# Kernel tuning notes

Hardware: AMD Instinct MI355X
Metric: run time of the kernel (lower is better)

The kernel has to match this reference:

```python
import jax, jax.numpy as jnp
import numpy as np

D = 1024
H = 16
HD = D // H
FFN = D * 2
EPS = 1e-5


def _layernorm(x, g, b):
    mu = jnp.mean(x, axis=-1, keepdims=True)
    var = jnp.var(x, axis=-1, keepdims=True)
    return (x - mu) * jax.lax.rsqrt(var + EPS) * g + b


def setup_inputs() -> dict:
    key = jax.random.key(0)
    ks = jax.random.split(key, 12)
    s = 1.0 / np.sqrt(D)
    inp = {
        "x": jax.random.normal(ks[0], (2, 2048, D), dtype=jnp.float32),
        "Wq": jax.random.normal(ks[1], (D, D), dtype=jnp.float32) * s,
        "bq": jnp.zeros((D,), jnp.float32),
        "Wk": jax.random.normal(ks[2], (D, D), dtype=jnp.float32) * s,
        "bk": jnp.zeros((D,), jnp.float32),
        "Wv": jax.random.normal(ks[3], (D, D), dtype=jnp.float32) * s,
        "bv": jnp.zeros((D,), jnp.float32),
        "Wo": jax.random.normal(ks[4], (D, D), dtype=jnp.float32) * s,
        "bo": jnp.zeros((D,), jnp.float32),
        "g1": jnp.ones((D,), jnp.float32),
        "b1": jnp.zeros((D,), jnp.float32),
        "W_ff1": jax.random.normal(ks[5], (D, FFN), dtype=jnp.float32) * s,
        "b_ff1": jnp.zeros((FFN,), jnp.float32),
        "W_ff2": jax.random.normal(ks[6], (FFN, D), dtype=jnp.float32) * (1.0 / np.sqrt(FFN)),
        "b_ff2": jnp.zeros((D,), jnp.float32),
        "g2": jnp.ones((D,), jnp.float32),
        "b2": jnp.zeros((D,), jnp.float32),
    }
    return inp


def reference(x, Wq, bq, Wk, bk, Wv, bv, Wo, bo, g1, b1, W_ff1, b_ff1, W_ff2, b_ff2, g2, b2):
    B, S, _ = x.shape
    # QKV projections -> [B, H, S, HD]
    def split_heads(t):
        return t.reshape(B, S, H, HD).transpose(0, 2, 1, 3)
    Q = split_heads(x @ Wq + bq)
    K = split_heads(x @ Wk + bk)
    V = split_heads(x @ Wv + bv)
    scores = jnp.einsum('bhqd,bhkd->bhqk', Q, K) / np.sqrt(HD).astype(np.float32)
    attn = jax.nn.softmax(scores, axis=-1)  # dropout = identity in eval
    ctx = jnp.einsum('bhqk,bhkd->bhqd', attn, V)
    ctx = ctx.transpose(0, 2, 1, 3).reshape(B, S, D)
    x = _layernorm(x + ctx @ Wo + bo, g1, b1)
    h = jax.nn.gelu(x @ W_ff1 + b_ff1, approximate=False)
    x = _layernorm(x + h @ W_ff2 + b_ff2, g2, b2)
    return x
```

## Files before the change

kernel.cpp:

```cpp
#include <hip/hip_runtime.h>

#define SEQ 2048
#define NTOK 4096
#define DM 1024
#define LDQK 3072

typedef __attribute__((ext_vector_type(4))) float f32x4;
typedef __attribute__((ext_vector_type(8))) short short8;
typedef __attribute__((ext_vector_type(4))) short short4v;

__device__ __forceinline__ short f2bf(float f) {
  union { float f; unsigned u; } x; x.f = f;
  unsigned r = x.u + 0x7fffu + ((x.u >> 16) & 1u);
  return (short)(r >> 16);
}

__device__ __forceinline__ float bf2f(short s) {
  union { unsigned u; float f; } x;
  x.u = ((unsigned)(unsigned short)s) << 16;
  return x.f;
}

__device__ __forceinline__ void async_load16(const void* g, void* l) {
  __builtin_amdgcn_global_load_lds(
      (const __attribute__((address_space(1))) void*)g,
      (__attribute__((address_space(3))) void*)l, 16, 0, 0);
}

__global__ void __launch_bounds__(256) prep_all(
    const float* __restrict__ Wq, const float* __restrict__ Wk,
    const float* __restrict__ Wv, const float* __restrict__ Wo,
    const float* __restrict__ Wf1, const float* __restrict__ Wf2,
    const float* __restrict__ x,
    short* __restrict__ Wqkv, short* __restrict__ Wto,
    short* __restrict__ Wtf1, short* __restrict__ Wtf2,
    short* __restrict__ xb) {
  const int z = blockIdx.z;
  const int tx = threadIdx.x, ty = threadIdx.y;
  if (z == 6) {
    int blk = blockIdx.y * 64 + blockIdx.x;
    int i = blk * 256 + ty * 32 + tx;
    f32x4 v = ((const f32x4*)x)[i];
    short4v o;
#pragma unroll
    for (int j = 0; j < 4; ++j) o[j] = f2bf(v[j]);
    ((short4v*)xb)[i] = o;
    return;
  }
  const float* in;
  short* out;
  int K, N;
  switch (z) {
    case 0: in = Wq;  out = Wqkv;               K = 1024; N = 1024; break;
    case 1: in = Wk;  out = Wqkv + 1024 * 1024; K = 1024; N = 1024; break;
    case 2: in = Wv;  out = Wqkv + 2048 * 1024; K = 1024; N = 1024; break;
    case 3: in = Wo;  out = Wto;                K = 1024; N = 1024; break;
    case 4: in = Wf1; out = Wtf1;               K = 1024; N = 2048; break;
    default: in = Wf2; out = Wtf2;              K = 2048; N = 1024; break;
  }
  if (blockIdx.x * 32 >= N || blockIdx.y * 32 >= K) return;
  __shared__ float t[32][33];
  const int n = blockIdx.x * 32 + tx;
#pragma unroll
  for (int i = 0; i < 4; ++i) {
    int k = blockIdx.y * 32 + ty + i * 8;
    t[ty + i * 8][tx] = in[(size_t)k * N + n];
  }
  __syncthreads();
  const int k2 = blockIdx.y * 32 + tx;
#pragma unroll
  for (int i = 0; i < 4; ++i) {
    int n2 = blockIdx.x * 32 + ty + i * 8;
    out[(size_t)n2 * K + k2] = f2bf(t[tx][ty + i * 8]);
  }
}

template <int EPI, bool TRIPLE, bool DBUF>
__global__ void __launch_bounds__(256, 2) gemm_bt(
    const short* __restrict__ A, const short* __restrict__ Bt,
    const float* __restrict__ b0, const float* __restrict__ b1,
    const float* __restrict__ b2, void* __restrict__ Cout,
    short* __restrict__ VtOut, int M, int N, int K) {
  __shared__ __align__(16) short As[DBUF ? 2 * 128 * 64 : 128 * 64];
  __shared__ __align__(16) short Bs[DBUF ? 2 * 128 * 64 : 128 * 64];
  const int w = threadIdx.x >> 6, lane = threadIdx.x & 63;
  const int hi = lane >> 4, lo = lane & 15;
  const int bm = blockIdx.y, bn = blockIdx.x;
  const int wr = w >> 1, wc = w & 1;
  f32x4 acc[4][4] = {};
  const int nkt = K >> 6;

  auto stage = [&](int kt, int buf) {
#pragma unroll
    for (int j = 0; j < 4; ++j) {
      int c = (j * 4 + w) * 64 + lane;
      int r = c >> 3;
      int scc = (c & 7) ^ (r & 7);
      async_load16(A + (size_t)(bm * 128 + r) * K + kt * 64 + scc * 8,
                   &As[buf * (128 * 64) + (j * 4 + w) * 512]);
      async_load16(Bt + (size_t)(bn * 128 + r) * K + kt * 64 + scc * 8,
                   &Bs[buf * (128 * 64) + (j * 4 + w) * 512]);
    }
  };

  if (DBUF) {
    stage(0, 0);
    __syncthreads();
  }

  for (int kt = 0; kt < nkt; ++kt) {
    int buf = 0;
    if (DBUF) {
      buf = kt & 1;
      if (kt + 1 < nkt) stage(kt + 1, buf ^ 1);
    } else {
      stage(kt, 0);
      __syncthreads();
    }
#pragma unroll
    for (int ks = 0; ks < 2; ++ks) {
      short8 af[4], bf[4];
#pragma unroll
      for (int m = 0; m < 4; ++m) {
        int row = wr * 64 + m * 16 + lo;
        int ch = (ks * 4 + hi) ^ (row & 7);
        af[m] = *(const short8*)(&As[buf * (128 * 64) + row * 64 + ch * 8]);
      }
#pragma unroll
      for (int n = 0; n < 4; ++n) {
        int row = wc * 64 + n * 16 + lo;
        int ch = (ks * 4 + hi) ^ (row & 7);
        bf[n] = *(const short8*)(&Bs[buf * (128 * 64) + row * 64 + ch * 8]);
      }
#pragma unroll
      for (int m = 0; m < 4; ++m)
#pragma unroll
        for (int n = 0; n < 4; ++n)
          acc[m][n] = __builtin_amdgcn_mfma_f32_16x16x32_bf16(af[m], bf[n], acc[m][n], 0, 0, 0);
    }
    __syncthreads();
  }
  const float* bp = b0;
  if (TRIPLE) { int r = bn >> 3; bp = (r == 0) ? b0 : ((r == 1) ? b1 : b2); }
  const int colb = bn * 128 + wc * 64 + lo;
  if (TRIPLE && bn >= 16) {
#pragma unroll
    for (int m = 0; m < 4; ++m) {
      int row0 = bm * 128 + wr * 64 + m * 16 + hi * 4;
      int bb = row0 >> 11, ss = row0 & 2047;
#pragma unroll
      for (int n = 0; n < 4; ++n) {
        int col = colb + n * 16;
        int vdim = col - 2048;
        int hh = vdim >> 6, dd = vdim & 63;
        float bs = bp[vdim];
        short4v t;
#pragma unroll
        for (int j = 0; j < 4; ++j) t[j] = f2bf(acc[m][n][j] + bs);
        *(short4v*)&VtOut[((size_t)(bb * 16 + hh) * 64 + dd) * SEQ + ss] = t;
      }
    }
    return;
  }
#pragma unroll
  for (int m = 0; m < 4; ++m) {
    int row0 = bm * 128 + wr * 64 + m * 16 + hi * 4;
#pragma unroll
    for (int n = 0; n < 4; ++n) {
      int col = colb + n * 16;
      float bs = bp[TRIPLE ? (col & 1023) : col];
#pragma unroll
      for (int j = 0; j < 4; ++j) {
        float v = acc[m][n][j] + bs;
        if (EPI == 1) v = 0.5f * v * (1.f + erff(v * 0.70710678f));
        ((short*)Cout)[(size_t)(row0 + j) * N + col] = f2bf(v);
      }
    }
  }
}

__global__ void __launch_bounds__(256, 2) gemm_n64(
    const short* __restrict__ A, const short* __restrict__ Bt,
    const float* __restrict__ b0, const short* __restrict__ resid,
    short* __restrict__ Cout, int M, int N, int K) {
  __shared__ __align__(16) short As[2][128 * 64];
  __shared__ __align__(16) short Bs[2][64 * 64];
  const int w = threadIdx.x >> 6, lane = threadIdx.x & 63;
  const int hi = lane >> 4, lo = lane & 15;
  const int bm = blockIdx.y, bn = blockIdx.x;
  const int wr = w >> 1, wc = w & 1;
  f32x4 acc[4][2] = {};
  const int nkt = K >> 6;

  auto stage = [&](int kt, int buf) {
#pragma unroll
    for (int j = 0; j < 4; ++j) {
      int c = (j * 4 + w) * 64 + lane;
      int r = c >> 3;
      int scc = (c & 7) ^ (r & 7);
      async_load16(A + (size_t)(bm * 128 + r) * K + kt * 64 + scc * 8,
                   &As[buf][(j * 4 + w) * 512]);
    }
#pragma unroll
    for (int j = 0; j < 2; ++j) {
      int c = j * 256 + w * 64 + lane;
      int r = c >> 3;
      int scc = (c & 7) ^ (r & 7);
      async_load16(Bt + (size_t)(bn * 64 + r) * K + kt * 64 + scc * 8,
                   &Bs[buf][(j * 256 + w * 64) * 8]);
    }
  };

  stage(0, 0);
  __syncthreads();

  for (int kt = 0; kt < nkt; ++kt) {
    const int buf = kt & 1;
    if (kt + 1 < nkt) stage(kt + 1, buf ^ 1);
#pragma unroll
    for (int ks = 0; ks < 2; ++ks) {
      short8 af[4], bf[2];
#pragma unroll
      for (int m = 0; m < 4; ++m) {
        int row = wr * 64 + m * 16 + lo;
        int ch = (ks * 4 + hi) ^ (row & 7);
        af[m] = *(const short8*)(&As[buf][row * 64 + ch * 8]);
      }
#pragma unroll
      for (int n = 0; n < 2; ++n) {
        int row = wc * 32 + n * 16 + lo;
        int ch = (ks * 4 + hi) ^ (row & 7);
        bf[n] = *(const short8*)(&Bs[buf][row * 64 + ch * 8]);
      }
#pragma unroll
      for (int m = 0; m < 4; ++m)
#pragma unroll
        for (int n = 0; n < 2; ++n)
          acc[m][n] = __builtin_amdgcn_mfma_f32_16x16x32_bf16(af[m], bf[n], acc[m][n], 0, 0, 0);
    }
    __syncthreads();
  }
  const int colb = bn * 64 + wc * 32 + lo;
#pragma unroll
  for (int m = 0; m < 4; ++m) {
    int row0 = bm * 128 + wr * 64 + m * 16 + hi * 4;
#pragma unroll
    for (int n = 0; n < 2; ++n) {
      int col = colb + n * 16;
      float bs = b0[col];
#pragma unroll
      for (int j = 0; j < 4; ++j) {
        size_t idx = (size_t)(row0 + j) * N + col;
        Cout[idx] = f2bf(acc[m][n][j] + bs + bf2f(resid[idx]));
      }
    }
  }
}

__global__ void __launch_bounds__(256, 2) attn_kernel(
    const short* __restrict__ Qb, const short* __restrict__ Kb,
    const short* __restrict__ Vt, short* __restrict__ ctx) {
  const int w = threadIdx.x >> 6, lane = threadIdx.x & 63;
  const int hi = lane >> 4, lo = lane & 15;
  const int tid = threadIdx.x;
  const int L = blockIdx.x;
  const int W = (L & 7) * 128 + (L >> 3);
  const int qt = W & 31, bh = W >> 5;
  const int b = bh >> 4, h = bh & 15;
  const int qbase = qt * 64 + w * 16;
  const float C = 0.18033688f;

  __shared__ __align__(16) short Ks[2][64 * 64];
  __shared__ __align__(16) short Vs[2][64 * 64];
  __shared__ __align__(16) short P[4][16 * 64];

  const short* qp = Qb + (size_t)(b * SEQ + qbase + lo) * LDQK + h * 64;
  short8 bq[2];
#pragma unroll
  for (int c = 0; c < 2; ++c)
    bq[c] = *(const short8*)(qp + c * 32 + hi * 8);

  const short* kb = Kb + (size_t)(b * SEQ) * LDQK + h * 64;
  const short* vb = Vt + (size_t)bh * 64 * SEQ;

  auto stage = [&](int kt, int buf) {
    const short* kg = kb + (size_t)(kt * 64) * LDQK;
#pragma unroll
    for (int i = 0; i < 2; ++i) {
      int c = i * 256 + tid;
      int r = c >> 3, scc = (c & 7) ^ (r & 7);
      async_load16(kg + (size_t)r * LDQK + scc * 8,
                   &Ks[buf][(i * 256 + w * 64) * 8]);
    }
    const short* vg = vb + kt * 64;
#pragma unroll
    for (int i = 0; i < 2; ++i) {
      int c = i * 256 + tid;
      int r = c >> 3, sc2 = (c & 7) ^ (r & 7);
      async_load16(vg + (size_t)r * SEQ + sc2 * 8,
                   &Vs[buf][(i * 256 + w * 64) * 8]);
    }
  };

  stage(0, 0);
  __syncthreads();

  f32x4 o[4] = {};
  float lacc = 0.f;
  const int x7 = lo & 7;

  for (int kt = 0; kt < SEQ / 64; ++kt) {
    const int buf = kt & 1;
    if (kt + 1 < SEQ / 64) stage(kt + 1, buf ^ 1);

    f32x4 s[4] = {};
#pragma unroll
    for (int g = 0; g < 4; ++g) {
      const short* kr = &Ks[buf][(g * 16 + lo) * 64];
      short8 ka0 = *(const short8*)(kr + ((hi) ^ x7) * 8);
      short8 ka1 = *(const short8*)(kr + ((4 + hi) ^ x7) * 8);
      s[g] = __builtin_amdgcn_mfma_f32_16x16x32_bf16(ka0, bq[0], s[g], 0, 0, 0);
      s[g] = __builtin_amdgcn_mfma_f32_16x16x32_bf16(ka1, bq[1], s[g], 0, 0, 0);
    }
    short8 vv[2][4];
#pragma unroll
    for (int ks = 0; ks < 2; ++ks)
#pragma unroll
      for (int a = 0; a < 4; ++a)
        vv[ks][a] = *(const short8*)(&Vs[buf][(a * 16 + lo) * 64 + (((ks * 4 + hi) ^ x7) * 8)]);

    float rsg[4];
    short* pbase = &P[w][0];
#pragma unroll
    for (int g = 0; g < 4; ++g) {
      float p0 = exp2f(s[g][0] * C);
      float p1 = exp2f(s[g][1] * C);
      float p2 = exp2f(s[g][2] * C);
      float p3 = exp2f(s[g][3] * C);
      rsg[g] = (p0 + p1) + (p2 + p3);
      unsigned w0, w1;
      asm("v_cvt_pk_bf16_f32 %0, %1, %2" : "=v"(w0) : "v"(p0), "v"(p1));
      asm("v_cvt_pk_bf16_f32 %0, %1, %2" : "=v"(w1) : "v"(p2), "v"(p3));
      union { unsigned uu[2]; short4v s4; } cv;
      cv.uu[0] = w0; cv.uu[1] = w1;
      int pc = (2 * g + (hi >> 1)) ^ x7;
      *(short4v*)(pbase + lo * 64 + pc * 8 + (hi & 1) * 4) = cv.s4;
    }
#pragma unroll
    for (int ks = 0; ks < 2; ++ks) {
      int pc = (ks * 4 + hi) ^ x7;
      short8 pa = *(const short8*)(pbase + lo * 64 + pc * 8);
#pragma unroll
      for (int a = 0; a < 4; ++a)
        o[a] = __builtin_amdgcn_mfma_f32_16x16x32_bf16(pa, vv[ks][a], o[a], 0, 0, 0);
    }
    lacc += (rsg[0] + rsg[1]) + (rsg[2] + rsg[3]);
    __syncthreads();
  }
  lacc += __shfl_xor(lacc, 16);
  lacc += __shfl_xor(lacc, 32);
#pragma unroll
  for (int j = 0; j < 4; ++j) {
    float lj = __shfl(lacc, hi * 4 + j);
    float inv = 1.f / lj;
    int row = qbase + hi * 4 + j;
#pragma unroll
    for (int a = 0; a < 4; ++a)
      ctx[(size_t)(b * SEQ + row) * DM + h * 64 + a * 16 + lo] = f2bf(o[a][j] * inv);
  }
}

__global__ void __launch_bounds__(256) ln_bf16(
    const short* __restrict__ in, const float* __restrict__ g,
    const float* __restrict__ beta, float* __restrict__ outf,
    short* __restrict__ outb) {
  const int row = blockIdx.x;
  const int t = threadIdx.x;
  const size_t base = (size_t)row * DM;
  short4v iv = ((const short4v*)(in + base))[t];
  f32x4 v;
#pragma unroll
  for (int j = 0; j < 4; ++j) v[j] = bf2f(iv[j]);
  float s = v[0] + v[1] + v[2] + v[3];
  float s2 = v[0] * v[0] + v[1] * v[1] + v[2] * v[2] + v[3] * v[3];
#pragma unroll
  for (int off = 1; off < 64; off <<= 1) {
    s += __shfl_xor(s, off);
    s2 += __shfl_xor(s2, off);
  }
  __shared__ float rs[4], rs2[4];
  if ((t & 63) == 0) { rs[t >> 6] = s; rs2[t >> 6] = s2; }
  __syncthreads();
  s = rs[0] + rs[1] + rs[2] + rs[3];
  s2 = rs2[0] + rs2[1] + rs2[2] + rs2[3];
  float mu = s * (1.f / DM);
  float var = s2 * (1.f / DM) - mu * mu;
  float rstd = rsqrtf(var + 1e-5f);
  f32x4 gv = ((const f32x4*)g)[t];
  f32x4 bv = ((const f32x4*)beta)[t];
  f32x4 ov;
#pragma unroll
  for (int j = 0; j < 4; ++j) ov[j] = (v[j] - mu) * rstd * gv[j] + bv[j];
  if (outf) ((f32x4*)(outf + base))[t] = ov;
  if (outb) {
    short4v sb;
#pragma unroll
    for (int j = 0; j < 4; ++j) sb[j] = f2bf(ov[j]);
    ((short4v*)(outb + base))[t] = sb;
  }
}

extern "C" void kernel_launch(void* const* d_in, const int* in_sizes, int n_in,
                              void* d_out, int out_size, void* d_ws, size_t ws_size,
                              hipStream_t stream) {
  (void)in_sizes; (void)n_in; (void)out_size; (void)ws_size;
  const float* x   = (const float*)d_in[0];
  const float* Wq  = (const float*)d_in[1];
  const float* bq  = (const float*)d_in[2];
  const float* Wk  = (const float*)d_in[3];
  const float* bk  = (const float*)d_in[4];
  const float* Wv  = (const float*)d_in[5];
  const float* bv  = (const float*)d_in[6];
  const float* Wo  = (const float*)d_in[7];
  const float* bo  = (const float*)d_in[8];
  const float* g1  = (const float*)d_in[9];
  const float* b1  = (const float*)d_in[10];
  const float* Wf1 = (const float*)d_in[11];
  const float* bf1 = (const float*)d_in[12];
  const float* Wf2 = (const float*)d_in[13];
  const float* bf2 = (const float*)d_in[14];
  const float* g2  = (const float*)d_in[15];
  const float* b2  = (const float*)d_in[16];

  char* ws = (char*)d_ws;
  const size_t MB = 1u << 20;
  short* Wqkv = (short*)(ws + 0 * MB);
  short* Wto  = (short*)(ws + 6 * MB);
  short* Wtf1 = (short*)(ws + 8 * MB);
  short* Wtf2 = (short*)(ws + 12 * MB);
  short* xb   = (short*)(ws + 16 * MB);
  short* QKV  = (short*)(ws + 24 * MB);
  short* Vt   = (short*)(ws + 48 * MB);
  short* ctxb = (short*)(ws + 56 * MB);
  short* aout = (short*)(ws + 64 * MB);
  short* x1b  = (short*)(ws + 72 * MB);
  short* hb   = QKV;
  short* ffo  = (short*)(ws + 48 * MB);

  prep_all<<<dim3(64, 64, 7), dim3(32, 8), 0, stream>>>(
      Wq, Wk, Wv, Wo, Wf1, Wf2, x, Wqkv, Wto, Wtf1, Wtf2, xb);

  gemm_bt<0, true, false><<<dim3(24, 32), 256, 0, stream>>>(
      xb, Wqkv, bq, bk, bv, QKV, Vt, NTOK, 3072, 1024);

  attn_kernel<<<dim3(1024), 256, 0, stream>>>(QKV, QKV + 1024, Vt, ctxb);

  gemm_n64<<<dim3(16, 32), 256, 0, stream>>>(ctxb, Wto, bo, xb, aout, NTOK, 1024, 1024);
  ln_bf16<<<4096, 256, 0, stream>>>(aout, g1, b1, nullptr, x1b);
  gemm_bt<1, false, true><<<dim3(16, 32), 256, 0, stream>>>(
      x1b, Wtf1, bf1, bf1, bf1, hb, nullptr, NTOK, 2048, 1024);
  gemm_n64<<<dim3(16, 32), 256, 0, stream>>>(hb, Wtf2, bf2, x1b, ffo, NTOK, 1024, 2048);
  ln_bf16<<<4096, 256, 0, stream>>>(ffo, g2, b2, (float*)d_out, nullptr);
}
```

Baseline: 215.6 us.

## Use 128x256 QKV GEMM tile with 512 threads and add MFMA priority hints in attention

Replaces the generic QKV GEMM with a dedicated kernel that runs 8 waves per block and computes a 128x256 output tile, cutting the grid from 768 to 384 blocks and raising reuse of each A tile. The kernel keeps single buffering with a synchronise after every K step. It also raises wave priority around the MFMA sections of the attention loop, so matrix work is favoured over the exp and softmax packing phase. The QKV tile change risks lower occupancy and leaves global-load latency exposed, since loads are not overlapped with compute.

```diff
diff --git a/kernel.cpp b/kernel.cpp
--- a/kernel.cpp
+++ b/kernel.cpp
@@ -75,12 +75,91 @@
   }
 }
 
-template <int EPI, bool TRIPLE, bool DBUF>
+__global__ void __launch_bounds__(512, 2) gemm_qkv8(
+    const short* __restrict__ A, const short* __restrict__ Bt,
+    const float* __restrict__ bq, const float* __restrict__ bk,
+    const float* __restrict__ bv, short* __restrict__ Cout,
+    short* __restrict__ VtOut) {
+  __shared__ __align__(16) short As[128 * 64];
+  __shared__ __align__(16) short Bs[256 * 64];
+  const int tid = threadIdx.x;
+  const int w = tid >> 6, lane = tid & 63;
+  const int hi = lane >> 4, lo = lane & 15;
+  const int bx = blockIdx.x, bm = blockIdx.y;
+  const int wr = w >> 2, wc = w & 3;
+  f32x4 acc[4][4] = {};
+
+  for (int kt = 0; kt < 16; ++kt) {
+#pragma unroll
+    for (int i = 0; i < 2; ++i) {
+      int c = i * 512 + tid;
+      int r = c >> 3, scc = (c & 7) ^ (r & 7);
+      async_load16(A + (size_t)(bm * 128 + r) * 1024 + kt * 64 + scc * 8,
+                   &As[(i * 8 + w) * 512]);
+    }
+#pragma unroll
+    for (int i = 0; i < 4; ++i) {
+      int c = i * 512 + tid;
+      int r = c >> 3, scc = (c & 7) ^ (r & 7);
+      async_load16(Bt + (size_t)(bx * 256 + r) * 1024 + kt * 64 + scc * 8,
+                   &Bs[(i * 8 + w) * 512]);
+    }
+    __syncthreads();
+#pragma unroll
+    for (int ks = 0; ks < 2; ++ks) {
+      short8 af[4], bf[4];
+#pragma unroll
+      for (int m = 0; m < 4; ++m) {
+        int row = wr * 64 + m * 16 + lo;
+        int ch = (ks * 4 + hi) ^ (row & 7);
+        af[m] = *(const short8*)(&As[row * 64 + ch * 8]);
+      }
+#pragma unroll
+      for (int n = 0; n < 4; ++n) {
+        int row = wc * 64 + n * 16 + lo;
+        int ch = (ks * 4 + hi) ^ (row & 7);
+        bf[n] = *(const short8*)(&Bs[row * 64 + ch * 8]);
+      }
+#pragma unroll
+      for (int m = 0; m < 4; ++m)
+#pragma unroll
+        for (int n = 0; n < 4; ++n)
+          acc[m][n] = __builtin_amdgcn_mfma_f32_16x16x32_bf16(af[m], bf[n], acc[m][n], 0, 0, 0);
+    }
+    __syncthreads();
+  }
+  const int colb = bx * 256 + wc * 64 + lo;
+#pragma unroll
+  for (int m = 0; m < 4; ++m) {
+    int row0 = bm * 128 + wr * 64 + m * 16 + hi * 4;
+#pragma unroll
+    for (int n = 0; n < 4; ++n) {
+      int col = colb + n * 16;
+      int r3 = col >> 10;
+      const float* bp = (r3 == 0) ? bq : ((r3 == 1) ? bk : bv);
+      float bs = bp[col & 1023];
+      if (r3 == 2) {
+        int vdim = col - 2048;
+        int hh = vdim >> 6, dd = vdim & 63;
+        int bb = row0 >> 11, ss = row0 & 2047;
+        short4v t;
+#pragma unroll
+        for (int j = 0; j < 4; ++j) t[j] = f2bf(acc[m][n][j] + bs);
+        *(short4v*)&VtOut[((size_t)(bb * 16 + hh) * 64 + dd) * SEQ + ss] = t;
+      } else {
+#pragma unroll
+        for (int j = 0; j < 4; ++j)
+          Cout[(size_t)(row0 + j) * LDQK + col] = f2bf(acc[m][n][j] + bs);
+      }
+    }
+  }
+}
+
+template <int EPI, bool DBUF>
 __global__ void __launch_bounds__(256, 2) gemm_bt(
     const short* __restrict__ A, const short* __restrict__ Bt,
-    const float* __restrict__ b0, const float* __restrict__ b1,
-    const float* __restrict__ b2, void* __restrict__ Cout,
-    short* __restrict__ VtOut, int M, int N, int K) {
+    const float* __restrict__ b0, void* __restrict__ Cout,
+    int M, int N, int K) {
   __shared__ __align__(16) short As[DBUF ? 2 * 128 * 64 : 128 * 64];
   __shared__ __align__(16) short Bs[DBUF ? 2 * 128 * 64 : 128 * 64];
   const int w = threadIdx.x >> 6, lane = threadIdx.x & 63;
@@ -140,35 +219,14 @@
     }
     __syncthreads();
   }
-  const float* bp = b0;
-  if (TRIPLE) { int r = bn >> 3; bp = (r == 0) ? b0 : ((r == 1) ? b1 : b2); }
   const int colb = bn * 128 + wc * 64 + lo;
-  if (TRIPLE && bn >= 16) {
-#pragma unroll
-    for (int m = 0; m < 4; ++m) {
-      int row0 = bm * 128 + wr * 64 + m * 16 + hi * 4;
-      int bb = row0 >> 11, ss = row0 & 2047;
-#pragma unroll
-      for (int n = 0; n < 4; ++n) {
-        int col = colb + n * 16;
-        int vdim = col - 2048;
-        int hh = vdim >> 6, dd = vdim & 63;
-        float bs = bp[vdim];
-        short4v t;
-#pragma unroll
-        for (int j = 0; j < 4; ++j) t[j] = f2bf(acc[m][n][j] + bs);
-        *(short4v*)&VtOut[((size_t)(bb * 16 + hh) * 64 + dd) * SEQ + ss] = t;
-      }
-    }
-    return;
-  }
 #pragma unroll
   for (int m = 0; m < 4; ++m) {
     int row0 = bm * 128 + wr * 64 + m * 16 + hi * 4;
 #pragma unroll
     for (int n = 0; n < 4; ++n) {
       int col = colb + n * 16;
-      float bs = bp[TRIPLE ? (col & 1023) : col];
+      float bs = b0[col];
 #pragma unroll
       for (int j = 0; j < 4; ++j) {
         float v = acc[m][n][j] + bs;
@@ -314,6 +372,7 @@
     if (kt + 1 < SEQ / 64) stage(kt + 1, buf ^ 1);
 
     f32x4 s[4] = {};
+    __builtin_amdgcn_s_setprio(1);
 #pragma unroll
     for (int g = 0; g < 4; ++g) {
       const short* kr = &Ks[buf][(g * 16 + lo) * 64];
@@ -322,6 +381,7 @@
       s[g] = __builtin_amdgcn_mfma_f32_16x16x32_bf16(ka0, bq[0], s[g], 0, 0, 0);
       s[g] = __builtin_amdgcn_mfma_f32_16x16x32_bf16(ka1, bq[1], s[g], 0, 0, 0);
     }
+    __builtin_amdgcn_s_setprio(0);
     short8 vv[2][4];
 #pragma unroll
     for (int ks = 0; ks < 2; ++ks)
@@ -346,6 +406,7 @@
       int pc = (2 * g + (hi >> 1)) ^ x7;
       *(short4v*)(pbase + lo * 64 + pc * 8 + (hi & 1) * 4) = cv.s4;
     }
+    __builtin_amdgcn_s_setprio(1);
 #pragma unroll
     for (int ks = 0; ks < 2; ++ks) {
       int pc = (ks * 4 + hi) ^ x7;
@@ -354,6 +415,7 @@
       for (int a = 0; a < 4; ++a)
         o[a] = __builtin_amdgcn_mfma_f32_16x16x32_bf16(pa, vv[ks][a], o[a], 0, 0, 0);
     }
+    __builtin_amdgcn_s_setprio(0);
     lacc += (rsg[0] + rsg[1]) + (rsg[2] + rsg[3]);
     __syncthreads();
   }
@@ -450,15 +512,14 @@
   prep_all<<<dim3(64, 64, 7), dim3(32, 8), 0, stream>>>(
       Wq, Wk, Wv, Wo, Wf1, Wf2, x, Wqkv, Wto, Wtf1, Wtf2, xb);
 
-  gemm_bt<0, true, false><<<dim3(24, 32), 256, 0, stream>>>(
-      xb, Wqkv, bq, bk, bv, QKV, Vt, NTOK, 3072, 1024);
+  gemm_qkv8<<<dim3(12, 32), 512, 0, stream>>>(xb, Wqkv, bq, bk, bv, QKV, Vt);
 
   attn_kernel<<<dim3(1024), 256, 0, stream>>>(QKV, QKV + 1024, Vt, ctxb);
 
   gemm_n64<<<dim3(16, 32), 256, 0, stream>>>(ctxb, Wto, bo, xb, aout, NTOK, 1024, 1024);
   ln_bf16<<<4096, 256, 0, stream>>>(aout, g1, b1, nullptr, x1b);
-  gemm_bt<1, false, true><<<dim3(16, 32), 256, 0, stream>>>(
-      x1b, Wtf1, bf1, bf1, bf1, hb, nullptr, NTOK, 2048, 1024);
+  gemm_bt<1, true><<<dim3(16, 32), 256, 0, stream>>>(
+      x1b, Wtf1, bf1, hb, NTOK, 2048, 1024);
   gemm_n64<<<dim3(16, 32), 256, 0, stream>>>(hb, Wtf2, bf2, x1b, ffo, NTOK, 1024, 2048);
   ln_bf16<<<4096, 256, 0, stream>>>(ffo, g2, b2, (float*)d_out, nullptr);
 }
```

New measurement: 206.5 us. 1.04x faster.
